# Performance work log

Measured on AMD Instinct MI355X. Metric: run time of the kernel, lower is better.

## Reference

```python
import jax, jax.numpy as jnp
import numpy as np

GROUP_SIZE = 64
BITS = 4
VALS_PER_WORD = 32 // BITS  # 8 nibbles per uint32


def setup_inputs() -> dict:
    key = jax.random.key(0)
    ks = jax.random.split(key, 7)
    B, S, I, O = 4, 2048, 4096, 4096
    G = I // GROUP_SIZE
    x = jax.random.normal(ks[0], (B, S, I), dtype=jnp.float32)
    channel_scale = jax.random.uniform(ks[1], (1, 1, I), dtype=jnp.float32, minval=0.5, maxval=1.5)
    # packed int4 weights: random uint32 words
    qweight = jax.random.randint(ks[2], (O, I // VALS_PER_WORD), 0, 2147483647, dtype=jnp.int32).astype(jnp.uint32)
    q_perm = jax.random.permutation(ks[3], I).astype(jnp.int32)
    scales = jax.random.uniform(ks[4], (O, G), dtype=jnp.float32, minval=0.001, maxval=0.02)
    zeros = jax.random.normal(ks[5], (O, G), dtype=jnp.float32) * 0.05
    bias = jax.random.normal(ks[6], (O,), dtype=jnp.float32) * 0.02
    return {"x": x, "channel_scale": channel_scale, "qweight": qweight,
            "q_perm": q_perm, "scales": scales, "zeros": zeros, "bias": bias}


def _dequantize(qweight, scales, zeros):
    # qweight: (O, I/8) uint32 -> nibbles little-endian within each word
    O, packed = qweight.shape
    shifts = (jnp.arange(VALS_PER_WORD, dtype=jnp.uint32) * BITS)  # (8,)
    wq = (qweight[:, :, None] >> shifts[None, None, :]) & jnp.uint32((1 << BITS) - 1)
    wq = wq.reshape(O, packed * VALS_PER_WORD).astype(jnp.float32)  # (O, I)
    # mlx dequantize: w = wq * scale + bias(zeros), per group of GROUP_SIZE along input dim
    s = jnp.repeat(scales, GROUP_SIZE, axis=1)  # (O, I)
    z = jnp.repeat(zeros, GROUP_SIZE, axis=1)   # (O, I)
    return wq * s + z


def reference(x, channel_scale, qweight, q_perm, scales, zeros, bias):
    # per-channel scale
    x = x * channel_scale
    # optional permute gather along feature axis
    x = jnp.take(x, q_perm, axis=-1)
    # group-wise int4 dequant matmul (transpose=True: out = x @ W^T)
    W = _dequantize(qweight, scales, zeros)  # (O, I)
    out = jnp.einsum('bsi,oi->bso', x, W)
    return out + bias
```

## Files before the change

### kernel.cpp

```cpp
#include <hip/hip_runtime.h>

typedef unsigned int u32;
typedef unsigned char u8;

#define M_DIM 8192
#define K_DIM 4096
#define N_DIM 4096
#define GROUPS 64

typedef int intx4 __attribute__((ext_vector_type(4)));

__device__ __forceinline__ void gload_lds16(const void* g, void* l) {
  __builtin_amdgcn_global_load_lds(
      (const __attribute__((address_space(1))) void*)g,
      (__attribute__((address_space(3))) void*)l, 16, 0, 0);
}

__device__ __forceinline__ u32 pack4(const float* v, float inv) {
  u32 r = 0;
#pragma unroll
  for (int i = 0; i < 4; ++i) {
    int q = (int)__builtin_rintf(v[i] * inv);
    q = q > 127 ? 127 : (q < -127 ? -127 : q);
    r |= ((u32)(u8)(char)q) << (8 * i);
  }
  return r;
}

__global__ __launch_bounds__(256) void prep_all(
    const float* __restrict__ x, const float* __restrict__ cs,
    const u32* __restrict__ qw, const int* __restrict__ perm,
    const float* __restrict__ scales, const float* __restrict__ zeros,
    u8* __restrict__ xq, u8* __restrict__ wq,
    float* __restrict__ sx, float* __restrict__ sw) {
  __shared__ float rowbuf[K_DIM];
  __shared__ float red[4];
  const int t = threadIdx.x;
  if (blockIdx.x < N_DIM) {
    const int base = t * 16;
    const int o = blockIdx.x;
    const u32* qrow = qw + (size_t)o * (K_DIM / 8);
    const float s = scales[o * GROUPS + (t >> 2)];
    const float z = zeros[o * GROUPS + (t >> 2)];
    uint2 w = *(const uint2*)(qrow + 2 * t);
    int4 p0 = *(const int4*)(perm + base + 0);
    int4 p1 = *(const int4*)(perm + base + 4);
    int4 p2 = *(const int4*)(perm + base + 8);
    int4 p3 = *(const int4*)(perm + base + 12);
    float v[16];
    float amax = 0.f;
#pragma unroll
    for (int n = 0; n < 8; ++n) {
      v[n]     = (float)((w.x >> (4 * n)) & 15u) * s + z;
      v[8 + n] = (float)((w.y >> (4 * n)) & 15u) * s + z;
      amax = fmaxf(amax, fmaxf(fabsf(v[n]), fabsf(v[8 + n])));
    }
    rowbuf[p0.x] = v[0];  rowbuf[p0.y] = v[1];
    rowbuf[p0.z] = v[2];  rowbuf[p0.w] = v[3];
    rowbuf[p1.x] = v[4];  rowbuf[p1.y] = v[5];
    rowbuf[p1.z] = v[6];  rowbuf[p1.w] = v[7];
    rowbuf[p2.x] = v[8];  rowbuf[p2.y] = v[9];
    rowbuf[p2.z] = v[10]; rowbuf[p2.w] = v[11];
    rowbuf[p3.x] = v[12]; rowbuf[p3.y] = v[13];
    rowbuf[p3.z] = v[14]; rowbuf[p3.w] = v[15];
#pragma unroll
    for (int off = 32; off; off >>= 1)
      amax = fmaxf(amax, __shfl_xor(amax, off, 64));
    if ((t & 63) == 0) red[t >> 6] = amax;
    __syncthreads();
    amax = fmaxf(fmaxf(red[0], red[1]), fmaxf(red[2], red[3]));
    amax = fmaxf(amax, 1e-20f);
    const float inv = 127.0f / amax;
    uint4 p;
    p.x = pack4(rowbuf + base + 0, inv);
    p.y = pack4(rowbuf + base + 4, inv);
    p.z = pack4(rowbuf + base + 8, inv);
    p.w = pack4(rowbuf + base + 12, inv);
    *(uint4*)(wq + (size_t)o * K_DIM + base) = p;
    if (t == 0) sw[o] = amax * (1.0f / 127.0f);
  } else {
    const int wave = t >> 6, lane = t & 63;
    const size_t m = (size_t)(blockIdx.x - N_DIM) * 4 + wave;
    const float* xr = x + m * K_DIM;
    float v[64];
    float amax = 0.f;
#pragma unroll
    for (int j = 0; j < 4; ++j) {
      const int col = j * 1024 + lane * 16;
#pragma unroll
      for (int u = 0; u < 4; ++u) {
        float4 xv = *(const float4*)(xr + col + u * 4);
        float4 cv = *(const float4*)(cs + col + u * 4);
        float* vp = v + j * 16 + u * 4;
        vp[0] = xv.x * cv.x;
        vp[1] = xv.y * cv.y;
        vp[2] = xv.z * cv.z;
        vp[3] = xv.w * cv.w;
        amax = fmaxf(amax, fmaxf(fmaxf(fabsf(vp[0]), fabsf(vp[1])),
                                 fmaxf(fabsf(vp[2]), fabsf(vp[3]))));
      }
    }
#pragma unroll
    for (int off = 32; off; off >>= 1)
      amax = fmaxf(amax, __shfl_xor(amax, off, 64));
    amax = fmaxf(amax, 1e-20f);
    const float inv = 127.0f / amax;
#pragma unroll
    for (int j = 0; j < 4; ++j) {
      uint4 p;
      p.x = pack4(v + j * 16 + 0, inv);
      p.y = pack4(v + j * 16 + 4, inv);
      p.z = pack4(v + j * 16 + 8, inv);
      p.w = pack4(v + j * 16 + 12, inv);
      *(uint4*)(xq + m * K_DIM + j * 1024 + lane * 16) = p;
    }
    if (lane == 0) sx[m] = amax * (1.0f / 127.0f);
  }
}

#define BM 128
#define BN 128
#define BK 64
#define KTILES (K_DIM / BK)

__global__ __launch_bounds__(256, 2) void gemm_i8(
    const u8* __restrict__ A, const u8* __restrict__ B,
    const float* __restrict__ sx, const float* __restrict__ sw,
    const float* __restrict__ bias, float* __restrict__ out) {
  __shared__ __align__(16) u8 As[3][BM * BK];
  __shared__ __align__(16) u8 Bs[3][BN * BK];
  const int tid = threadIdx.x;
  const int lane = tid & 63;
  const int wave = tid >> 6;
  const int wm = wave >> 1;
  const int wn = wave & 1;
  const int q = lane >> 4, lr = lane & 15;
  const int qs = q ^ ((lr >> 1) & 3);

  const int wg = blockIdx.x;
  const int swzwg = (wg & 7) * 256 + (wg >> 3);
  const int blockN = (swzwg & 31) * BN;
  const int blockM = (swzwg >> 5) * BM;

  const char* Abase = (const char*)(A + (size_t)blockM * K_DIM);
  const char* Bbase = (const char*)(B + (size_t)blockN * K_DIM);

  const int c0 = tid, c1 = tid + 256;
  const int kc0 = (c0 & 3) ^ ((c0 >> 3) & 3);
  const int kc1 = (c1 & 3) ^ ((c1 >> 3) & 3);
  const size_t gOff0 = (size_t)(c0 >> 2) * K_DIM + kc0 * 16;
  const size_t gOff1 = (size_t)(c1 >> 2) * K_DIM + kc1 * 16;
  const int dOff0 = c0 * 16, dOff1 = c1 * 16;

  const int aoff = (wm * 64 + lr) * 64 + qs * 16;
  const int boff = (wn * 64 + lr) * 64 + qs * 16;

  intx4 acc[4][4];
#pragma unroll
  for (int i = 0; i < 4; ++i)
#pragma unroll
    for (int j = 0; j < 4; ++j) acc[i][j] = (intx4)0;

  auto stage = [&](int t, int b) {
    const size_t koff = (size_t)t * BK;
    gload_lds16(Abase + gOff0 + koff, &As[b][dOff0]);
    gload_lds16(Abase + gOff1 + koff, &As[b][dOff1]);
    gload_lds16(Bbase + gOff0 + koff, &Bs[b][dOff0]);
    gload_lds16(Bbase + gOff1 + koff, &Bs[b][dOff1]);
  };

  stage(0, 0);
  stage(1, 1);
  asm volatile("s_waitcnt vmcnt(4)" ::: "memory");
  asm volatile("s_barrier" ::: "memory");

  int bc = 0, bs = 2;
  for (int t = 0; t < KTILES; ++t) {
    if (t + 2 < KTILES) stage(t + 2, bs);

    const u8* Ab = &As[bc][0];
    const u8* Bb = &Bs[bc][0];
    intx4 af[4], bf[4];
#pragma unroll
    for (int mi = 0; mi < 4; ++mi)
      af[mi] = *(const intx4*)(Ab + aoff + mi * 1024);
#pragma unroll
    for (int ni = 0; ni < 4; ++ni)
      bf[ni] = *(const intx4*)(Bb + boff + ni * 1024);

    __builtin_amdgcn_s_setprio(1);
#pragma unroll
    for (int mi = 0; mi < 4; ++mi)
#pragma unroll
      for (int ni = 0; ni < 4; ++ni)
        acc[mi][ni] = __builtin_amdgcn_mfma_i32_16x16x64_i8(
            af[mi], bf[ni], acc[mi][ni], 0, 0, 0);
    __builtin_amdgcn_s_setprio(0);

    if (t + 2 < KTILES) {
      asm volatile("s_waitcnt vmcnt(4)" ::: "memory");
    } else if (t + 1 < KTILES) {
      asm volatile("s_waitcnt vmcnt(0)" ::: "memory");
    }
    if (t + 1 < KTILES) asm volatile("s_barrier" ::: "memory");

    bc = (bc == 2) ? 0 : bc + 1;
    bs = (bs == 2) ? 0 : bs + 1;
  }

#pragma unroll
  for (int ni = 0; ni < 4; ++ni) {
    const int col = blockN + wn * 64 + ni * 16 + lr;
    const float swv = sw[col];
    const float bv = bias[col];
#pragma unroll
    for (int mi = 0; mi < 4; ++mi) {
      const int row0 = blockM + wm * 64 + mi * 16 + q * 4;
#pragma unroll
      for (int r = 0; r < 4; ++r) {
        const float s = sx[row0 + r] * swv;
        out[(size_t)(row0 + r) * N_DIM + col] = (float)acc[mi][ni][r] * s + bv;
      }
    }
  }
}

extern "C" void kernel_launch(void* const* d_in, const int* in_sizes, int n_in,
                              void* d_out, int out_size, void* d_ws, size_t ws_size,
                              hipStream_t stream) {
  const float* x      = (const float*)d_in[0];
  const float* cs     = (const float*)d_in[1];
  const u32*   qw     = (const u32*)d_in[2];
  const int*   perm   = (const int*)d_in[3];
  const float* scales = (const float*)d_in[4];
  const float* zeros  = (const float*)d_in[5];
  const float* bias   = (const float*)d_in[6];
  float* out = (float*)d_out;

  u8* xq = (u8*)d_ws;
  u8* wq = xq + (size_t)M_DIM * K_DIM;
  float* sx = (float*)(wq + (size_t)N_DIM * K_DIM);
  float* sw = sx + M_DIM;

  hipLaunchKernelGGL(prep_all, dim3(N_DIM + M_DIM / 4), dim3(256), 0, stream,
                     x, cs, qw, perm, scales, zeros, xq, wq, sx, sw);
  hipLaunchKernelGGL(gemm_i8, dim3((M_DIM / BM) * (N_DIM / BN)), dim3(256), 0,
                     stream, xq, wq, sx, sw, bias, out);
}
```

Baseline: 404.9 us.

## Enlarge GEMM M-tile to 256 and load A fragments directly into registers

```diff
diff --git a/kernel.cpp b/kernel.cpp
--- a/kernel.cpp
+++ b/kernel.cpp
@@ -118,7 +118,7 @@
   }
 }
 
-#define BM 128
+#define BM 256
 #define BN 128
 #define BK 64
 #define KTILES (K_DIM / BK)
@@ -127,7 +127,6 @@
     const u8* __restrict__ A, const u8* __restrict__ B,
     const float* __restrict__ sx, const float* __restrict__ sw,
     const float* __restrict__ bias, float* __restrict__ out) {
-  __shared__ __align__(16) u8 As[3][BM * BK];
   __shared__ __align__(16) u8 Bs[3][BN * BK];
   const int tid = threadIdx.x;
   const int lane = tid & 63;
@@ -138,75 +137,86 @@
   const int qs = q ^ ((lr >> 1) & 3);
 
   const int wg = blockIdx.x;
-  const int swzwg = (wg & 7) * 256 + (wg >> 3);
+  const int swzwg = (wg & 7) * 128 + (wg >> 3);
   const int blockN = (swzwg & 31) * BN;
   const int blockM = (swzwg >> 5) * BM;
 
-  const char* Abase = (const char*)(A + (size_t)blockM * K_DIM);
   const char* Bbase = (const char*)(B + (size_t)blockN * K_DIM);
+  const char* Aptr = (const char*)A +
+      ((size_t)(blockM + wm * 128 + lr) * K_DIM + q * 16);
 
   const int c0 = tid, c1 = tid + 256;
-  const int kc0 = (c0 & 3) ^ ((c0 >> 3) & 3);
-  const int kc1 = (c1 & 3) ^ ((c1 >> 3) & 3);
-  const size_t gOff0 = (size_t)(c0 >> 2) * K_DIM + kc0 * 16;
-  const size_t gOff1 = (size_t)(c1 >> 2) * K_DIM + kc1 * 16;
-  const int dOff0 = c0 * 16, dOff1 = c1 * 16;
-
-  const int aoff = (wm * 64 + lr) * 64 + qs * 16;
+  const int kcB0 = (c0 & 3) ^ ((c0 >> 3) & 3);
+  const int kcB1 = (c1 & 3) ^ ((c1 >> 3) & 3);
+  const size_t gOffB0 = (size_t)(c0 >> 2) * K_DIM + kcB0 * 16;
+  const size_t gOffB1 = (size_t)(c1 >> 2) * K_DIM + kcB1 * 16;
+  const int dOffB0 = c0 * 16, dOffB1 = c1 * 16;
+
   const int boff = (wn * 64 + lr) * 64 + qs * 16;
 
-  intx4 acc[4][4];
-#pragma unroll
-  for (int i = 0; i < 4; ++i)
+  intx4 acc[8][4];
+#pragma unroll
+  for (int i = 0; i < 8; ++i)
 #pragma unroll
     for (int j = 0; j < 4; ++j) acc[i][j] = (intx4)0;
 
-  auto stage = [&](int t, int b) {
-    const size_t koff = (size_t)t * BK;
-    gload_lds16(Abase + gOff0 + koff, &As[b][dOff0]);
-    gload_lds16(Abase + gOff1 + koff, &As[b][dOff1]);
-    gload_lds16(Bbase + gOff0 + koff, &Bs[b][dOff0]);
-    gload_lds16(Bbase + gOff1 + koff, &Bs[b][dOff1]);
-  };
-
-  stage(0, 0);
-  stage(1, 1);
-  asm volatile("s_waitcnt vmcnt(4)" ::: "memory");
-  asm volatile("s_barrier" ::: "memory");
-
-  int bc = 0, bs = 2;
-  for (int t = 0; t < KTILES; ++t) {
-    if (t + 2 < KTILES) stage(t + 2, bs);
-
-    const u8* Ab = &As[bc][0];
-    const u8* Bb = &Bs[bc][0];
-    intx4 af[4], bf[4];
-#pragma unroll
-    for (int mi = 0; mi < 4; ++mi)
-      af[mi] = *(const intx4*)(Ab + aoff + mi * 1024);
-#pragma unroll
-    for (int ni = 0; ni < 4; ++ni)
-      bf[ni] = *(const intx4*)(Bb + boff + ni * 1024);
-
-    __builtin_amdgcn_s_setprio(1);
-#pragma unroll
-    for (int mi = 0; mi < 4; ++mi)
-#pragma unroll
-      for (int ni = 0; ni < 4; ++ni)
-        acc[mi][ni] = __builtin_amdgcn_mfma_i32_16x16x64_i8(
-            af[mi], bf[ni], acc[mi][ni], 0, 0, 0);
-    __builtin_amdgcn_s_setprio(0);
-
-    if (t + 2 < KTILES) {
-      asm volatile("s_waitcnt vmcnt(4)" ::: "memory");
-    } else if (t + 1 < KTILES) {
-      asm volatile("s_waitcnt vmcnt(0)" ::: "memory");
-    }
-    if (t + 1 < KTILES) asm volatile("s_barrier" ::: "memory");
-
-    bc = (bc == 2) ? 0 : bc + 1;
-    bs = (bs == 2) ? 0 : bs + 1;
-  }
+  intx4 a0[8], a1[8];
+
+#define STAGE_B(T) do {                                          \
+    const size_t koff_ = (size_t)(T) * BK;                       \
+    u8* Bw_ = &Bs[(T) % 3][0];                                   \
+    gload_lds16(Bbase + gOffB0 + koff_, Bw_ + dOffB0);           \
+    gload_lds16(Bbase + gOffB1 + koff_, Bw_ + dOffB1);           \
+  } while (0)
+
+#define LOAD_A(T, AR) do {                                       \
+    const char* ap_ = Aptr + (size_t)(T) * BK;                   \
+    _Pragma("unroll")                                            \
+    for (int mi = 0; mi < 8; ++mi)                               \
+      AR[mi] = *(const intx4*)(ap_ + mi * (16 * K_DIM));         \
+  } while (0)
+
+#define TILE(T, AUSE, DOSTAGE, ALOADT, ALOAD) do {               \
+    if (DOSTAGE) STAGE_B((T) + 2);                               \
+    if (ALOADT) LOAD_A((T) + 1, ALOAD);                          \
+    const u8* Bb_ = &Bs[(T) % 3][0];                             \
+    intx4 bf[4];                                                 \
+    _Pragma("unroll")                                            \
+    for (int ni = 0; ni < 4; ++ni)                               \
+      bf[ni] = *(const intx4*)(Bb_ + boff + ni * 1024);          \
+    _Pragma("unroll")                                            \
+    for (int mi = 0; mi < 8; ++mi)                               \
+      _Pragma("unroll")                                          \
+      for (int ni = 0; ni < 4; ++ni)                             \
+        acc[mi][ni] = __builtin_amdgcn_mfma_i32_16x16x64_i8(     \
+            AUSE[mi], bf[ni], acc[mi][ni], 0, 0, 0);             \
+  } while (0)
+
+#define VM10_BAR asm volatile("s_waitcnt vmcnt(10)\n\ts_barrier" ::: "memory")
+
+  STAGE_B(0);
+  STAGE_B(1);
+  LOAD_A(0, a0);
+  asm volatile("s_waitcnt vmcnt(0)\n\ts_barrier" ::: "memory");
+
+  for (int tt = 0; tt < KTILES - 4; tt += 2) {
+    TILE(tt, a0, 1, 1, a1);
+    VM10_BAR;
+    TILE(tt + 1, a1, 1, 1, a0);
+    VM10_BAR;
+  }
+  TILE(60, a0, 1, 1, a1);
+  VM10_BAR;
+  TILE(61, a1, 1, 1, a0);
+  VM10_BAR;
+  TILE(62, a0, 0, 1, a1);
+  asm volatile("s_waitcnt vmcnt(8)\n\ts_barrier" ::: "memory");
+  TILE(63, a1, 0, 0, a0);
+
+#undef STAGE_B
+#undef LOAD_A
+#undef TILE
+#undef VM10_BAR
 
 #pragma unroll
   for (int ni = 0; ni < 4; ++ni) {
@@ -214,8 +224,8 @@
     const float swv = sw[col];
     const float bv = bias[col];
 #pragma unroll
-    for (int mi = 0; mi < 4; ++mi) {
-      const int row0 = blockM + wm * 64 + mi * 16 + q * 4;
+    for (int mi = 0; mi < 8; ++mi) {
+      const int row0 = blockM + wm * 128 + mi * 16 + q * 4;
 #pragma unroll
       for (int r = 0; r < 4; ++r) {
         const float s = sx[row0 + r] * swv;
```

Result: slower. 523.8 us (+29.4%).
